# Performance work log

Hardware: AMD Instinct MI355X
Metric: run time of the kernel (lower is better)

The kernel has to match this reference:

```python
import jax, jax.numpy as jnp
import numpy as np

NUM_CLASSES = 1000
NUM_NODES = 1111  # 1000 leaves + 100 + 10 + 1 root
BATCH = 32768


def _build_hierarchy():
    """Deterministic 10-ary 3-level hierarchy standing in for heirachy_graph.p.

    Returns:
      A: [NUM_NODES, NUM_CLASSES] float32, A[n, l] = 1 if node n lies on leaf l's
         path to root (including leaf l itself). probs = outputs @ A.T reproduces
         the per-sample dict accumulation probs[node] += val.
      W: [NUM_CLASSES, NUM_NODES] float32 path-weight vectors:
         W[t, path[j]] += 2^-(j+1) for path root->t, plus the extra
         W[t, t] += 2^-len(path) term from the source.
    """
    parent = {}
    for l in range(1000):
        parent[l] = 1000 + l // 10
    for k in range(100):
        parent[1000 + k] = 1100 + k // 10
    for m in range(10):
        parent[1100 + m] = 1110
    parent[1110] = None

    A = np.zeros((NUM_NODES, NUM_CLASSES), dtype=np.float32)
    for l in range(NUM_CLASSES):
        node = l
        A[node, l] = 1.0
        while parent[node] is not None:
            node = parent[node]
            A[node, l] += 1.0

    W = np.zeros((NUM_CLASSES, NUM_NODES), dtype=np.float32)
    for t in range(NUM_CLASSES):
        path = [t]
        node = t
        while parent[node] is not None:
            node = parent[node]
            path = [node] + path
        for j, p in enumerate(path):
            W[t, p] += 2.0 ** (-(j + 1))
        W[t, t] += 2.0 ** (-len(path))  # extra target term in the source
    return A, W


def setup_inputs() -> dict:
    key = jax.random.key(0)
    k1, k2 = jax.random.split(key)
    outputs = jax.random.normal(k1, (BATCH, NUM_CLASSES), dtype=jnp.float32)
    target = jax.random.randint(k2, (BATCH,), 0, NUM_CLASSES, dtype=jnp.int64)
    A_np, W_np = _build_hierarchy()
    return {
        "outputs": outputs,
        "target": target,
        "A": jnp.asarray(A_np),
        "W": jnp.asarray(W_np),
    }


def reference(outputs, target, A, W):
    # probs[b, n] = sum over leaves l under node n of outputs[b, l]
    probs = outputs @ A.T                      # [B, NUM_NODES]
    w = W[target]                               # [B, NUM_NODES] gather per target
    win = jnp.einsum("bn,bn->b", probs, w)     # [B]
    return jnp.sum(1.0 - win)                  # scalar loss
```

## Files before the change

kernel.cpp:

```cpp
#include <hip/hip_runtime.h>


constexpr int BATCH   = 32768;
constexpr int NCLS    = 1000;
constexpr int N4      = BATCH * NCLS / 4;
constexpr int BLOCKS  = 2048;
constexpr int THREADS = 256;
constexpr int ROWS_PER_BLOCK = BATCH / BLOCKS;

__global__ __launch_bounds__(THREADS) void hloss_part(
    const float* __restrict__ outputs,
    const int*   __restrict__ target,
    float* __restrict__ partials)
{
    __shared__ float red[4];
    const int lane = threadIdx.x & 63;
    const int wid  = threadIdx.x >> 6;
    float win = 0.0f;

    {
        const int rowbase = blockIdx.x * ROWS_PER_BLOCK + wid * 4;
        const int h  = lane >> 5;
        const int ln = lane & 31;
        int tmine = 0;
        if (lane < 4) tmine = target[rowbase + lane];
        #pragma unroll
        for (int pass = 0; pass < 2; ++pass) {
            const int r = pass * 2 + h;
            const int t = __shfl(tmine, r, 64);
            const int b = rowbase + r;
            const int lo100 = (t / 100) * 100;
            const int lo10  = (t / 10)  * 10;
            if (ln < 25) {
                const int l0 = lo100 + ln * 4;
                const float4 v = *reinterpret_cast<const float4*>(
                    outputs + (size_t)b * NCLS + l0);
                const float xs[4] = {v.x, v.y, v.z, v.w};
                #pragma unroll
                for (int j = 0; j < 4; ++j) {
                    const int l = l0 + j;
                    float w = 0.25f;
                    if ((unsigned)(l - lo10) < 10u) w += 0.125f;
                    if (l == t)                     w += 0.125f;
                    win = fmaf(xs[j], w, win);
                }
            }
        }
    }

    {
        const float4* src = reinterpret_cast<const float4*>(outputs);
        const int tid    = blockIdx.x * THREADS + threadIdx.x;
        const int stride = BLOCKS * THREADS;
        float a0 = 0.f, a1 = 0.f, a2 = 0.f, a3 = 0.f;
        int i = tid;
        for (; i + 3 * stride < N4; i += 4 * stride) {
            const float4 v0 = src[i];
            const float4 v1 = src[i + stride];
            const float4 v2 = src[i + 2 * stride];
            const float4 v3 = src[i + 3 * stride];
            a0 += v0.x + v0.y + v0.z + v0.w;
            a1 += v1.x + v1.y + v1.z + v1.w;
            a2 += v2.x + v2.y + v2.z + v2.w;
            a3 += v3.x + v3.y + v3.z + v3.w;
        }
        for (; i < N4; i += stride) {
            const float4 v = src[i];
            a0 += v.x + v.y + v.z + v.w;
        }
        win = fmaf(0.5f, (a0 + a1) + (a2 + a3), win);
    }

    #pragma unroll
    for (int off = 32; off > 0; off >>= 1)
        win += __shfl_xor(win, off, 64);
    if (lane == 0) red[wid] = win;
    __syncthreads();
    if (threadIdx.x == 0)
        partials[blockIdx.x] = red[0] + red[1] + red[2] + red[3];
}

__global__ __launch_bounds__(THREADS) void hloss_final(
    const float* __restrict__ partials,
    float* __restrict__ out)
{
    __shared__ float red[4];
    const int lane = threadIdx.x & 63;
    const int wid  = threadIdx.x >> 6;
    float s = 0.0f;
    for (int i = threadIdx.x; i < BLOCKS; i += THREADS)
        s += partials[i];
    #pragma unroll
    for (int off = 32; off > 0; off >>= 1)
        s += __shfl_xor(s, off, 64);
    if (lane == 0) red[wid] = s;
    __syncthreads();
    if (threadIdx.x == 0)
        out[0] = (float)BATCH - (red[0] + red[1] + red[2] + red[3]);
}

extern "C" void kernel_launch(void* const* d_in, const int* in_sizes, int n_in,
                              void* d_out, int out_size, void* d_ws, size_t ws_size,
                              hipStream_t stream) {
    const float* outputs = (const float*)d_in[0];
    const int*   target  = (const int*)d_in[1];
    float* out      = (float*)d_out;
    float* partials = (float*)d_ws;

    hloss_part <<<dim3(BLOCKS), dim3(THREADS), 0, stream>>>(outputs, target, partials);
    hloss_final<<<dim3(1),      dim3(THREADS), 0, stream>>>(partials, out);
}
```

Before: 34.11 us.

## Fuse final reduction into main kernel via last-block atomic counter

Replaces the separate single-block final reduction kernel with a last-block-done pattern: each block writes its partial, fences, and bumps a global atomic counter, and the block that arrives last sums all partials and writes the loss. The streaming sum loop is rewritten with a compile-time trip count, fully unrolled, with a single guarded remainder load, and launch bounds now request 8 blocks per CU. This removes one kernel launch and its dependency gap but adds a memset launch to reset the counter, plus an atomic and fences per block.

```diff
diff --git a/kernel.cpp b/kernel.cpp
--- a/kernel.cpp
+++ b/kernel.cpp
@@ -7,13 +7,19 @@
 constexpr int BLOCKS  = 2048;
 constexpr int THREADS = 256;
 constexpr int ROWS_PER_BLOCK = BATCH / BLOCKS;
+constexpr int STRIDE  = BLOCKS * THREADS;
+constexpr int KFULL   = N4 / STRIDE;
+constexpr int NREM    = N4 - KFULL * STRIDE;
 
-__global__ __launch_bounds__(THREADS) void hloss_part(
+__global__ __launch_bounds__(THREADS, 8) void hloss(
     const float* __restrict__ outputs,
     const int*   __restrict__ target,
-    float* __restrict__ partials)
+    float*       __restrict__ partials,
+    unsigned*    __restrict__ counter,
+    float*       __restrict__ out)
 {
     __shared__ float red[4];
+    __shared__ int   lastflag;
     const int lane = threadIdx.x & 63;
     const int wid  = threadIdx.x >> 6;
     float win = 0.0f;
@@ -50,25 +56,18 @@
 
     {
         const float4* src = reinterpret_cast<const float4*>(outputs);
-        const int tid    = blockIdx.x * THREADS + threadIdx.x;
-        const int stride = BLOCKS * THREADS;
-        float a0 = 0.f, a1 = 0.f, a2 = 0.f, a3 = 0.f;
-        int i = tid;
-        for (; i + 3 * stride < N4; i += 4 * stride) {
-            const float4 v0 = src[i];
-            const float4 v1 = src[i + stride];
-            const float4 v2 = src[i + 2 * stride];
-            const float4 v3 = src[i + 3 * stride];
-            a0 += v0.x + v0.y + v0.z + v0.w;
-            a1 += v1.x + v1.y + v1.z + v1.w;
-            a2 += v2.x + v2.y + v2.z + v2.w;
-            a3 += v3.x + v3.y + v3.z + v3.w;
+        const int tid = blockIdx.x * THREADS + threadIdx.x;
+        float acc[4] = {0.f, 0.f, 0.f, 0.f};
+        #pragma unroll
+        for (int k = 0; k < KFULL; ++k) {
+            const float4 v = src[tid + k * STRIDE];
+            acc[k & 3] += (v.x + v.y) + (v.z + v.w);
         }
-        for (; i < N4; i += stride) {
-            const float4 v = src[i];
-            a0 += v.x + v.y + v.z + v.w;
+        if (tid < NREM) {
+            const float4 v = src[tid + KFULL * STRIDE];
+            acc[3] += (v.x + v.y) + (v.z + v.w);
         }
-        win = fmaf(0.5f, (a0 + a1) + (a2 + a3), win);
+        win = fmaf(0.5f, (acc[0] + acc[1]) + (acc[2] + acc[3]), win);
     }
 
     #pragma unroll
@@ -76,27 +75,32 @@
         win += __shfl_xor(win, off, 64);
     if (lane == 0) red[wid] = win;
     __syncthreads();
-    if (threadIdx.x == 0)
+
+    if (threadIdx.x == 0) {
         partials[blockIdx.x] = red[0] + red[1] + red[2] + red[3];
-}
+        __threadfence();
+        const unsigned old = atomicAdd(counter, 1u);
+        if (old == BLOCKS - 1) {
+            __threadfence();
+            lastflag = 1;
+        } else {
+            lastflag = 0;
+        }
+    }
+    __syncthreads();
 
-__global__ __launch_bounds__(THREADS) void hloss_final(
-    const float* __restrict__ partials,
-    float* __restrict__ out)
-{
-    __shared__ float red[4];
-    const int lane = threadIdx.x & 63;
-    const int wid  = threadIdx.x >> 6;
-    float s = 0.0f;
-    for (int i = threadIdx.x; i < BLOCKS; i += THREADS)
-        s += partials[i];
-    #pragma unroll
-    for (int off = 32; off > 0; off >>= 1)
-        s += __shfl_xor(s, off, 64);
-    if (lane == 0) red[wid] = s;
-    __syncthreads();
-    if (threadIdx.x == 0)
-        out[0] = (float)BATCH - (red[0] + red[1] + red[2] + red[3]);
+    if (lastflag) {
+        float s = 0.0f;
+        for (int i = threadIdx.x; i < BLOCKS; i += THREADS)
+            s += partials[i];
+        #pragma unroll
+        for (int off = 32; off > 0; off >>= 1)
+            s += __shfl_xor(s, off, 64);
+        if (lane == 0) red[wid] = s;
+        __syncthreads();
+        if (threadIdx.x == 0)
+            out[0] = (float)BATCH - ((red[0] + red[1]) + (red[2] + red[3]));
+    }
 }
 
 extern "C" void kernel_launch(void* const* d_in, const int* in_sizes, int n_in,
@@ -104,9 +108,12 @@
                               hipStream_t stream) {
     const float* outputs = (const float*)d_in[0];
     const int*   target  = (const int*)d_in[1];
-    float* out      = (float*)d_out;
-    float* partials = (float*)d_ws;
+    float*    out      = (float*)d_out;
+    unsigned* counter  = (unsigned*)d_ws;
+    float*    partials = (float*)((char*)d_ws + 1024);
 
-    hloss_part <<<dim3(BLOCKS), dim3(THREADS), 0, stream>>>(outputs, target, partials);
-    hloss_final<<<dim3(1),      dim3(THREADS), 0, stream>>>(partials, out);
+    hipMemsetAsync(d_ws, 0, 64, stream);
+
+    hloss<<<dim3(BLOCKS), dim3(THREADS), 0, stream>>>(
+        outputs, target, partials, counter, out);
 }
```

Result: slower. 98.75 us (+189.5%).
